# Optimization experiments

Measured on AMD Instinct MI355X. Metric: run time of the kernel, lower is better.

## Reference

```python
import jax, jax.numpy as jnp
import numpy as np

N, E = 20000, 320000
IN_DIM, H, C, L = 256, 128, 40, 3
EPS = 1e-5


def _ln(x, g, b):
    mu = jnp.mean(x, axis=-1, keepdims=True)
    var = jnp.mean(jnp.square(x - mu), axis=-1, keepdims=True)
    return (x - mu) * jax.lax.rsqrt(var + EPS) * g + b


def setup_inputs() -> dict:
    key = jax.random.key(0)
    ks = jax.random.split(key, 24)
    s = lambda *sh: 1.0 / np.sqrt(sh[-2] if len(sh) > 1 else sh[-1])
    inp = {
        "x": jax.random.normal(ks[0], (N, IN_DIM), jnp.float32),
        "edge_index": jax.random.randint(ks[1], (2, E), 0, N, jnp.int32),
        "proj_W": jax.random.normal(ks[2], (IN_DIM, H), jnp.float32) / np.sqrt(IN_DIM),
        "proj_b": jnp.zeros((H,), jnp.float32),
        "ln0_g": jnp.ones((H,), jnp.float32),
        "ln0_b": jnp.zeros((H,), jnp.float32),
        "sim_W1": jax.random.normal(ks[3], (L, 3 * H, H), jnp.float32) / np.sqrt(3 * H),
        "sim_b1": jnp.zeros((L, H), jnp.float32),
        "sim_W2": jax.random.normal(ks[4], (L, H, 1), jnp.float32) / np.sqrt(H),
        "sim_b2": jnp.zeros((L, 1), jnp.float32),
        "W_msg": jax.random.normal(ks[5], (L, H, H), jnp.float32) / np.sqrt(H),
        "W_upd": jax.random.normal(ks[6], (L, 2 * H, H), jnp.float32) / np.sqrt(2 * H),
        "b_upd": jnp.zeros((L, H), jnp.float32),
        "ln_g": jnp.ones((L, H), jnp.float32),
        "ln_b": jnp.zeros((L, H), jnp.float32),
        "cls_W1": jax.random.normal(ks[7], (H, H // 2), jnp.float32) / np.sqrt(H),
        "cls_b1": jnp.zeros((H // 2,), jnp.float32),
        "cls_W2": jax.random.normal(ks[8], (H // 2, C), jnp.float32) / np.sqrt(H // 2),
        "cls_b2": jnp.zeros((C,), jnp.float32),
    }
    return inp


def reference(x, edge_index, proj_W, proj_b, ln0_g, ln0_b, sim_W1, sim_b1,
              sim_W2, sim_b2, W_msg, W_upd, b_upd, ln_g, ln_b,
              cls_W1, cls_b1, cls_W2, cls_b2):
    n = x.shape[0]
    # add self loops
    loops = jnp.arange(n, dtype=edge_index.dtype)
    src = jnp.concatenate([edge_index[0], loops])
    dst = jnp.concatenate([edge_index[1], loops])

    h = jax.nn.relu(_ln(x @ proj_W + proj_b, ln0_g, ln0_b))  # (N,H); dropout=eval no-op

    for l in range(L):
        x_i = h[dst]                      # (E',H)
        x_j = h[src]                      # (E',H)
        sim_in = jnp.concatenate([x_i, x_j, jnp.abs(x_i - x_j)], axis=-1)  # (E',3H)
        hmid = jax.nn.relu(sim_in @ sim_W1[l] + sim_b1[l])
        score = jax.nn.sigmoid(hmid @ sim_W2[l] + sim_b2[l])  # (E',1)
        msg = x_j @ W_msg[l]              # (E',H)
        agg = jax.ops.segment_sum(score * msg, dst, num_segments=n)  # (N,H)
        upd = jnp.concatenate([h, agg], axis=-1) @ W_upd[l] + b_upd[l]
        upd = upd + h                     # residual (identity since in==out)
        h = jax.nn.relu(_ln(upd, ln_g[l], ln_b[l]))

    logits = jax.nn.relu(h @ cls_W1 + cls_b1) @ cls_W2 + cls_b2
    return logits
```

## Files before the change

### kernel.cpp

```cpp
#include <hip/hip_runtime.h>
#include <hip/hip_bf16.h>

#define HD 128
#define LN_EPS 1e-5f

typedef __attribute__((ext_vector_type(8))) short short8;
typedef __attribute__((ext_vector_type(4))) float f32x4;

__device__ __forceinline__ unsigned short f2bf(float f) {
    union { float f; unsigned u; } v; v.f = f;
    unsigned r = (v.u + 0x7fffu + ((v.u >> 16) & 1u)) >> 16;
    return (unsigned short)r;
}

__device__ __forceinline__ unsigned cvtpk(float lo, float hi) {
    unsigned r;
    asm("v_cvt_pk_bf16_f32 %0, %1, %2" : "=v"(r) : "v"(lo), "v"(hi));
    return r;
}
__device__ __forceinline__ unsigned cvtpk_abs(float lo, float hi) {
    unsigned r;
    asm("v_cvt_pk_bf16_f32 %0, abs(%1), abs(%2)" : "=v"(r) : "v"(lo), "v"(hi));
    return r;
}
__device__ __forceinline__ unsigned absd_bf2(unsigned a, unsigned b) {
    float alo = __uint_as_float(a << 16), ahi = __uint_as_float(a & 0xffff0000u);
    float blo = __uint_as_float(b << 16), bhi = __uint_as_float(b & 0xffff0000u);
    return cvtpk_abs(alo - blo, ahi - bhi);
}
__device__ __forceinline__ float bflo(unsigned u) { return __uint_as_float(u << 16); }
__device__ __forceinline__ float bfhi(unsigned u) { return __uint_as_float(u & 0xffff0000u); }

__device__ __forceinline__ float wave_sum_all(float v) {
    #pragma unroll
    for (int o = 32; o > 0; o >>= 1) v += __shfl_xor(v, o);
    return v;
}

__global__ __launch_bounds__(256) void w1bf_kernel(
    const float* __restrict__ W1, unsigned short* __restrict__ out, int total)
{
    int idx = blockIdx.x * 256 + threadIdx.x;
    if (idx >= total) return;
    int lw  = idx / 49152;
    int rem = idx - lw * 49152;
    int j  = rem & 7;
    int c  = (rem >> 3) & 15;
    int ks = (rem >> 7) & 3;
    int ct = (rem >> 9) & 7;
    int q  = rem >> 12;
    out[idx] = f2bf(W1[(size_t)lw * 49152 + (size_t)(q * 32 + ks * 8 + j) * 128 + ct * 16 + c]);
}

__global__ __launch_bounds__(256) void wcbf_kernel(
    const float* __restrict__ W_upd, const float* __restrict__ wcomb2,
    unsigned short* __restrict__ out, int total)
{
    int idx = blockIdx.x * 256 + threadIdx.x;
    if (idx >= total) return;
    int lw  = idx >> 15;
    int rem = idx & 32767;
    int j  = rem & 7;
    int c  = (rem >> 3) & 15;
    int ks = (rem >> 7) & 3;
    int ct = (rem >> 9) & 7;
    int q  = rem >> 12;
    int row = q * 32 + ks * 8 + j;
    int col = ct * 16 + c;
    float v = (row < 128) ? W_upd[(size_t)lw * 32768 + (size_t)row * 128 + col]
                          : wcomb2[(size_t)lw * 16384 + (size_t)(row - 128) * 128 + col];
    out[idx] = f2bf(v);
}

__global__ __launch_bounds__(256) void wmsg_gemm_kernel(
    const float* __restrict__ W_msg, const float* __restrict__ W_upd,
    float* __restrict__ wcomb2)
{
    __shared__ __align__(16) float rows[4][8][128];
    int l   = blockIdx.x >> 2;
    int blk = blockIdx.x & 3;
    const float* A = W_msg + (size_t)l * 16384;
    const float* W = W_upd + (size_t)l * 32768 + 16384;
    float* out = wcomb2 + (size_t)l * 16384;
    int tid = threadIdx.x, wv = tid >> 6, lane = tid & 63;
    int rbase = (blk * 4 + wv) * 8;
    int r = lane >> 3, seg = lane & 7;
    {
        const float2* p = (const float2*)(A + (size_t)(rbase + r) * 128 + seg * 16);
        float2* q = (float2*)&rows[wv][r][seg * 16];
        #pragma unroll
        for (int i = 0; i < 8; i++) q[i] = p[i];
    }
    asm volatile("s_waitcnt lgkmcnt(0)" ::: "memory");
    float2 acc[8];
    #pragma unroll
    for (int t = 0; t < 8; t++) acc[t] = make_float2(0.f, 0.f);
    for (int k = 0; k < 128; k += 4) {
        float2 w0 = *(const float2*)(W + (size_t)(k + 0) * 128 + 2 * lane);
        float2 w1 = *(const float2*)(W + (size_t)(k + 1) * 128 + 2 * lane);
        float2 w2 = *(const float2*)(W + (size_t)(k + 2) * 128 + 2 * lane);
        float2 w3 = *(const float2*)(W + (size_t)(k + 3) * 128 + 2 * lane);
        #pragma unroll
        for (int t = 0; t < 8; t++) {
            float4 a = *(const float4*)&rows[wv][t][k];
            acc[t].x = fmaf(a.x, w0.x, acc[t].x); acc[t].y = fmaf(a.x, w0.y, acc[t].y);
            acc[t].x = fmaf(a.y, w1.x, acc[t].x); acc[t].y = fmaf(a.y, w1.y, acc[t].y);
            acc[t].x = fmaf(a.z, w2.x, acc[t].x); acc[t].y = fmaf(a.z, w2.y, acc[t].y);
            acc[t].x = fmaf(a.w, w3.x, acc[t].x); acc[t].y = fmaf(a.w, w3.y, acc[t].y);
        }
    }
    #pragma unroll
    for (int t = 0; t < 8; t++)
        *(float2*)(out + (size_t)(rbase + t) * 128 + 2 * lane) = acc[t];
}

__global__ __launch_bounds__(256) void gemm_rows_kernel(
    const float* __restrict__ in0, int s0, const float* __restrict__ in1, int s1,
    const float* __restrict__ W, const float* __restrict__ bias,
    const float* __restrict__ res, const float* __restrict__ g,
    const float* __restrict__ bln, float* __restrict__ out,
    unsigned* __restrict__ out_bf, int N)
{
    __shared__ __align__(16) float rows[4][8][256];
    int tid = threadIdx.x, wv = tid >> 6, lane = tid & 63;
    int rbase = (blockIdx.x * 4 + wv) * 8;
    if (rbase >= N) return;
    int K = in1 ? 256 : 128;
    int r = lane >> 3, seg = lane & 7;
    int row = min(rbase + r, N - 1);
    {
        const float4* p = (const float4*)(in0 + (size_t)row * s0 + seg * 16);
        float4* q = (float4*)&rows[wv][r][seg * 16];
        #pragma unroll
        for (int i = 0; i < 4; i++) q[i] = p[i];
        if (in1) {
            const float4* p1 = (const float4*)(in1 + (size_t)row * s1 + seg * 16);
            float4* q1 = (float4*)&rows[wv][r][128 + seg * 16];
            #pragma unroll
            for (int i = 0; i < 4; i++) q1[i] = p1[i];
        }
    }
    asm volatile("s_waitcnt lgkmcnt(0)" ::: "memory");
    float2 acc[8];
    float2 bv = make_float2(0.f, 0.f);
    if (bias) bv = *(const float2*)(bias + 2 * lane);
    #pragma unroll
    for (int t = 0; t < 8; t++) acc[t] = bv;
    for (int k = 0; k < K; k += 4) {
        float2 w0 = *(const float2*)(W + (size_t)(k + 0) * 128 + 2 * lane);
        float2 w1 = *(const float2*)(W + (size_t)(k + 1) * 128 + 2 * lane);
        float2 w2 = *(const float2*)(W + (size_t)(k + 2) * 128 + 2 * lane);
        float2 w3 = *(const float2*)(W + (size_t)(k + 3) * 128 + 2 * lane);
        #pragma unroll
        for (int t = 0; t < 8; t++) {
            float4 a = *(const float4*)&rows[wv][t][k];
            acc[t].x = fmaf(a.x, w0.x, acc[t].x); acc[t].y = fmaf(a.x, w0.y, acc[t].y);
            acc[t].x = fmaf(a.y, w1.x, acc[t].x); acc[t].y = fmaf(a.y, w1.y, acc[t].y);
            acc[t].x = fmaf(a.z, w2.x, acc[t].x); acc[t].y = fmaf(a.z, w2.y, acc[t].y);
            acc[t].x = fmaf(a.w, w3.x, acc[t].x); acc[t].y = fmaf(a.w, w3.y, acc[t].y);
        }
    }
    if (res) {
        #pragma unroll
        for (int t = 0; t < 8; t++) {
            int rw = rbase + t;
            if (rw < N) {
                float2 rv = *(const float2*)(res + (size_t)rw * 128 + 2 * lane);
                acc[t].x += rv.x; acc[t].y += rv.y;
            }
        }
    }
    if (g) {
        float2 gv = *(const float2*)(g + 2 * lane);
        float2 lv = *(const float2*)(bln + 2 * lane);
        #pragma unroll
        for (int t = 0; t < 8; t++) {
            int rw = rbase + t;
            if (rw >= N) break;
            float s  = wave_sum_all(acc[t].x + acc[t].y);
            float s2 = wave_sum_all(acc[t].x * acc[t].x + acc[t].y * acc[t].y);
            float mu = s * (1.f / 128.f);
            float var = s2 * (1.f / 128.f) - mu * mu;
            float rs = rsqrtf(var + LN_EPS);
            float2 y;
            y.x = fmaxf((acc[t].x - mu) * rs * gv.x + lv.x, 0.f);
            y.y = fmaxf((acc[t].y - mu) * rs * gv.y + lv.y, 0.f);
            *(float2*)(out + (size_t)rw * 128 + 2 * lane) = y;
            if (out_bf) out_bf[(size_t)rw * 64 + lane] = cvtpk(y.x, y.y);
        }
    } else {
        #pragma unroll
        for (int t = 0; t < 8; t++) {
            int rw = rbase + t;
            if (rw < N) *(float2*)(out + (size_t)rw * 128 + 2 * lane) = acc[t];
        }
    }
}

__global__ __launch_bounds__(256) void hist_kernel(
    const int* __restrict__ dstA, int* __restrict__ cnt, int E, int Etot)
{
    for (int e = blockIdx.x * 256 + threadIdx.x; e < Etot; e += gridDim.x * 256) {
        int di = (e < E) ? dstA[e] : (e - E);
        atomicAdd(&cnt[di], 1);
    }
}

__global__ __launch_bounds__(256) void scan_kernel(
    const int* __restrict__ cnt, int* __restrict__ rowptr, int* __restrict__ cursor,
    int N, int Etot)
{
    __shared__ int ls[256];
    int t = threadIdx.x;
    int chunk = (N + 255) / 256;
    int lo = t * chunk, hi = min(lo + chunk, N);
    int s = 0;
    for (int i = lo; i < hi; i++) s += cnt[i];
    ls[t] = s;
    __syncthreads();
    for (int off = 1; off < 256; off <<= 1) {
        int v = (t >= off) ? ls[t - off] : 0;
        __syncthreads();
        ls[t] += v;
        __syncthreads();
    }
    int run = ls[t] - s;
    for (int i = lo; i < hi; i++) {
        rowptr[i] = run; cursor[i] = run;
        run += cnt[i];
    }
    if (t == 0) rowptr[N] = Etot;
}

__global__ __launch_bounds__(256) void scatter_kernel(
    const int* __restrict__ srcA, const int* __restrict__ dstA,
    int* __restrict__ cursor, int* __restrict__ esrc, int* __restrict__ edst,
    int E, int Etot)
{
    for (int e = blockIdx.x * 256 + threadIdx.x; e < Etot; e += gridDim.x * 256) {
        int si = (e < E) ? srcA[e] : (e - E);
        int di = (e < E) ? dstA[e] : (e - E);
        int pos = atomicAdd(&cursor[di], 1);
        esrc[pos] = si;
        edst[pos] = di;
    }
}

__global__ __launch_bounds__(256, 3) void edge_mfma_kernel(
    const unsigned* __restrict__ hbf,
    const int* __restrict__ esrc, const int* __restrict__ edst,
    const unsigned short* __restrict__ w1bf, const float* __restrict__ b1,
    const float* __restrict__ W2, const float* __restrict__ b2p,
    float* __restrict__ score, int Etot)
{
    __shared__ __align__(16) short sim[3][64][128];
    __shared__ float pl[4][64];
    int tid = threadIdx.x, wv = tid >> 6, lane = tid & 63;
    char* simb = (char*)sim;

    short8 wf[12][2];
    {
        int ks = lane >> 4, c = lane & 15;
        #pragma unroll
        for (int q = 0; q < 12; q++)
            #pragma unroll
            for (int n = 0; n < 2; n++) {
                int ct = wv * 2 + n;
                wf[q][n] = *(const short8*)(w1bf + (size_t)(((q * 8 + ct) * 4 + ks) * 128 + c * 8));
            }
    }
    float b1x = b1[wv * 32 + (lane & 15)],  b1y = b1[wv * 32 + 16 + (lane & 15)];
    float w2x = W2[wv * 32 + (lane & 15)],  w2y = W2[wv * 32 + 16 + (lane & 15)];
    float b2 = b2p[0];

    int nb = gridDim.x;
    int swz = (blockIdx.x & 7) * (nb >> 3) + (blockIdx.x >> 3);
    int ntiles = (Etot + 63) >> 6;
    int t0 = (int)(((long long)ntiles * swz) / nb);
    int t1 = (int)(((long long)ntiles * (swz + 1)) / nb);
    if (t0 >= t1) return;

    int el = tid >> 2, seg = tid & 3;
    int e_cur = min((t0 << 6) + el, Etot - 1);
    int si = esrc[e_cur];
    int di = edst[e_cur];

    for (int tile = t0; tile < t1; tile++) {
        const uint4* xi = (const uint4*)(hbf + (size_t)di * 64 + seg * 16);
        const uint4* xj = (const uint4*)(hbf + (size_t)si * 64 + seg * 16);
        uint4 a0 = xi[0], b0 = xj[0];
        uint4 a1 = xi[1], b1v = xj[1];
        uint4 a2 = xi[2], b2v = xj[2];
        uint4 a3 = xi[3], b3v = xj[3];
        {
            int nt = (tile + 1 < t1) ? (tile + 1) : tile;
            int en = min((nt << 6) + el, Etot - 1);
            si = esrc[en];
            di = edst[en];
        }
        {
            int rowoff = el * 256, sw = (el & 7) << 4;
            uint4 d0, d1, d2, d3;
            d0.x = absd_bf2(a0.x, b0.x);  d0.y = absd_bf2(a0.y, b0.y);
            d0.z = absd_bf2(a0.z, b0.z);  d0.w = absd_bf2(a0.w, b0.w);
            d1.x = absd_bf2(a1.x, b1v.x); d1.y = absd_bf2(a1.y, b1v.y);
            d1.z = absd_bf2(a1.z, b1v.z); d1.w = absd_bf2(a1.w, b1v.w);
            d2.x = absd_bf2(a2.x, b2v.x); d2.y = absd_bf2(a2.y, b2v.y);
            d2.z = absd_bf2(a2.z, b2v.z); d2.w = absd_bf2(a2.w, b2v.w);
            d3.x = absd_bf2(a3.x, b3v.x); d3.y = absd_bf2(a3.y, b3v.y);
            d3.z = absd_bf2(a3.z, b3v.z); d3.w = absd_bf2(a3.w, b3v.w);
            int o0 = rowoff + ((seg * 64 +  0) ^ sw);
            int o1 = rowoff + ((seg * 64 + 16) ^ sw);
            int o2 = rowoff + ((seg * 64 + 32) ^ sw);
            int o3 = rowoff + ((seg * 64 + 48) ^ sw);
            *(uint4*)(simb + o0)         = a0;  *(uint4*)(simb + o1)         = a1;
            *(uint4*)(simb + o2)         = a2;  *(uint4*)(simb + o3)         = a3;
            *(uint4*)(simb + 16384 + o0) = b0;  *(uint4*)(simb + 16384 + o1) = b1v;
            *(uint4*)(simb + 16384 + o2) = b2v; *(uint4*)(simb + 16384 + o3) = b3v;
            *(uint4*)(simb + 32768 + o0) = d0;  *(uint4*)(simb + 32768 + o1) = d1;
            *(uint4*)(simb + 32768 + o2) = d2;  *(uint4*)(simb + 32768 + o3) = d3;
        }
        __syncthreads();
        f32x4 acc[4][2];
        #pragma unroll
        for (int m = 0; m < 4; m++)
            #pragma unroll
            for (int n = 0; n < 2; n++)
                #pragma unroll
                for (int r = 0; r < 4; r++) acc[m][n][r] = 0.f;
        __builtin_amdgcn_s_setprio(1);
        #pragma unroll
        for (int q = 0; q < 12; q++) {
            int third = q >> 2;
            int kin = ((q & 3) * 64 + (lane >> 4) * 16);
            short8 af[4];
            #pragma unroll
            for (int m = 0; m < 4; m++) {
                int elr = m * 16 + (lane & 15);
                int addr = third * 16384 + elr * 256 + (kin ^ ((elr & 7) << 4));
                af[m] = *(const short8*)(simb + addr);
            }
            #pragma unroll
            for (int m = 0; m < 4; m++)
                #pragma unroll
                for (int n = 0; n < 2; n++)
                    acc[m][n] = __builtin_amdgcn_mfma_f32_16x16x32_bf16(af[m], wf[q][n], acc[m][n], 0, 0, 0);
        }
        __builtin_amdgcn_s_setprio(0);
        int ebase = tile << 6;
        #pragma unroll
        for (int m = 0; m < 4; m++) {
            #pragma unroll
            for (int r = 0; r < 4; r++) {
                float v = fmaxf(acc[m][0][r] + b1x, 0.f) * w2x
                        + fmaxf(acc[m][1][r] + b1y, 0.f) * w2y;
                v += __shfl_xor(v, 1); v += __shfl_xor(v, 2);
                v += __shfl_xor(v, 4); v += __shfl_xor(v, 8);
                if ((lane & 15) == 0) pl[wv][m * 16 + (lane >> 4) * 4 + r] = v;
            }
        }
        __syncthreads();
        if (tid < 64) {
            int e = ebase + tid;
            if (e < Etot) {
                float z = pl[0][tid] + pl[1][tid] + pl[2][tid] + pl[3][tid] + b2;
                score[e] = 1.f / (1.f + __expf(-z));
            }
        }
    }
}

__global__ __launch_bounds__(256) void gather_kernel(
    const int* __restrict__ rowptr, const int* __restrict__ esrc,
    const float* __restrict__ score, const unsigned* __restrict__ hbf,
    unsigned* __restrict__ paggbf, int N)
{
    int nb = gridDim.x;
    int bid = blockIdx.x;
    int swz = (bid & 7) * (nb >> 3) + (bid >> 3);
    int wvi = threadIdx.x >> 6, lane = threadIdx.x & 63;
    int node = swz * 4 + wvi;
    if (node >= N) return;
    int p0 = rowptr[node], p1 = rowptr[node + 1];
    int half = lane >> 5, l32 = lane & 31;
    const uint2* hb2 = (const uint2*)hbf;
    float4 c0 = make_float4(0.f, 0.f, 0.f, 0.f), c1 = c0, c2 = c0, c3 = c0;
    for (int base = p0; base < p1; base += 64) {
        int cnt = min(64, p1 - base);
        int sidx = 0; float sc = 0.f;
        if (lane < cnt) {
            sidx = esrc[base + lane];
            sc = score[base + lane];
        }
        for (int i = 0; i < cnt; i += 8) {
            int j0 = i + 0 + half, j1 = i + 2 + half, j2 = i + 4 + half, j3 = i + 6 + half;
            float s0 = __shfl(sc, j0), s1 = __shfl(sc, j1);
            float s2 = __shfl(sc, j2), s3 = __shfl(sc, j3);
            int r0 = __shfl(sidx, j0), r1 = __shfl(sidx, j1);
            int r2 = __shfl(sidx, j2), r3 = __shfl(sidx, j3);
            if (j0 >= cnt) s0 = 0.f;
            if (j1 >= cnt) s1 = 0.f;
            if (j2 >= cnt) s2 = 0.f;
            if (j3 >= cnt) s3 = 0.f;
            uint2 u0 = hb2[(size_t)r0 * 32 + l32];
            uint2 u1 = hb2[(size_t)r1 * 32 + l32];
            uint2 u2 = hb2[(size_t)r2 * 32 + l32];
            uint2 u3 = hb2[(size_t)r3 * 32 + l32];
            c0.x = fmaf(s0, bflo(u0.x), c0.x); c0.y = fmaf(s0, bfhi(u0.x), c0.y);
            c0.z = fmaf(s0, bflo(u0.y), c0.z); c0.w = fmaf(s0, bfhi(u0.y), c0.w);
            c1.x = fmaf(s1, bflo(u1.x), c1.x); c1.y = fmaf(s1, bfhi(u1.x), c1.y);
            c1.z = fmaf(s1, bflo(u1.y), c1.z); c1.w = fmaf(s1, bfhi(u1.y), c1.w);
            c2.x = fmaf(s2, bflo(u2.x), c2.x); c2.y = fmaf(s2, bfhi(u2.x), c2.y);
            c2.z = fmaf(s2, bflo(u2.y), c2.z); c2.w = fmaf(s2, bfhi(u2.y), c2.w);
            c3.x = fmaf(s3, bflo(u3.x), c3.x); c3.y = fmaf(s3, bfhi(u3.x), c3.y);
            c3.z = fmaf(s3, bflo(u3.y), c3.z); c3.w = fmaf(s3, bfhi(u3.y), c3.w);
        }
    }
    float4 t;
    t.x = (c0.x + c1.x) + (c2.x + c3.x);
    t.y = (c0.y + c1.y) + (c2.y + c3.y);
    t.z = (c0.z + c1.z) + (c2.z + c3.z);
    t.w = (c0.w + c1.w) + (c2.w + c3.w);
    t.x += __shfl_xor(t.x, 32);
    t.y += __shfl_xor(t.y, 32);
    t.z += __shfl_xor(t.z, 32);
    t.w += __shfl_xor(t.w, 32);
    if (half == 0) {
        uint2 o;
        o.x = cvtpk(t.x, t.y);
        o.y = cvtpk(t.z, t.w);
        ((uint2*)paggbf)[(size_t)node * 32 + l32] = o;
    }
}

__global__ __launch_bounds__(256, 3) void upd_mfma_kernel(
    const unsigned* __restrict__ hbf, const unsigned* __restrict__ paggbf,
    const float* __restrict__ hres,
    const unsigned short* __restrict__ wcbf,
    const float* __restrict__ bias, const float* __restrict__ g,
    const float* __restrict__ bln,
    float* __restrict__ hout, unsigned* __restrict__ hbf_out, int N)
{
    __shared__ float ps[4][64], pq[4][64];
    int tid = threadIdx.x, wv = tid >> 6, lane = tid & 63;
    int c = lane & 15, l16 = lane >> 4;
    int rbase = blockIdx.x * 64;
    if (rbase >= N) return;

    short8 wf[8][2];
    #pragma unroll
    for (int q = 0; q < 8; q++)
        #pragma unroll
        for (int n = 0; n < 2; n++) {
            int ct = wv * 2 + n;
            wf[q][n] = *(const short8*)(wcbf + (size_t)(((q * 8 + ct) * 4 + l16) * 128 + c * 8));
        }
    float g0  = g[wv * 32 + c],    g1  = g[wv * 32 + 16 + c];
    float lb0 = bln[wv * 32 + c],  lb1 = bln[wv * 32 + 16 + c];
    float bs0 = bias[wv * 32 + c], bs1 = bias[wv * 32 + 16 + c];

    f32x4 acc[4][2];
    #pragma unroll
    for (int m = 0; m < 4; m++)
        #pragma unroll
        for (int n = 0; n < 2; n++)
            #pragma unroll
            for (int r = 0; r < 4; r++) acc[m][n][r] = 0.f;

    int arow[4];
    #pragma unroll
    for (int m = 0; m < 4; m++) arow[m] = min(rbase + m * 16 + c, N - 1);

    #pragma unroll
    for (int q = 0; q < 8; q++) {
        const unsigned* src = (q < 4) ? hbf : paggbf;
        int qq = (q < 4) ? q : q - 4;
        short8 af[4];
        #pragma unroll
        for (int m = 0; m < 4; m++)
            af[m] = *(const short8*)(src + (size_t)arow[m] * 64 + qq * 16 + l16 * 4);
        #pragma unroll
        for (int m = 0; m < 4; m++)
            #pragma unroll
            for (int n = 0; n < 2; n++)
                acc[m][n] = __builtin_amdgcn_mfma_f32_16x16x32_bf16(af[m], wf[q][n], acc[m][n], 0, 0, 0);
    }

    #pragma unroll
    for (int m = 0; m < 4; m++) {
        #pragma unroll
        for (int r = 0; r < 4; r++) {
            int rit = m * 16 + l16 * 4 + r;
            int rowc = min(rbase + rit, N - 1);
            float v0 = acc[m][0][r] + bs0 + hres[(size_t)rowc * 128 + wv * 32 + c];
            float v1 = acc[m][1][r] + bs1 + hres[(size_t)rowc * 128 + wv * 32 + 16 + c];
            acc[m][0][r] = v0; acc[m][1][r] = v1;
            float s = v0 + v1, sq = v0 * v0 + v1 * v1;
            s  += __shfl_xor(s, 1);  s  += __shfl_xor(s, 2);  s  += __shfl_xor(s, 4);  s  += __shfl_xor(s, 8);
            sq += __shfl_xor(sq, 1); sq += __shfl_xor(sq, 2); sq += __shfl_xor(sq, 4); sq += __shfl_xor(sq, 8);
            if (c == 0) { ps[wv][rit] = s; pq[wv][rit] = sq; }
        }
    }
    __syncthreads();
    #pragma unroll
    for (int m = 0; m < 4; m++) {
        #pragma unroll
        for (int r = 0; r < 4; r++) {
            int rit = m * 16 + l16 * 4 + r;
            int row = rbase + rit;
            float s  = (ps[0][rit] + ps[1][rit]) + (ps[2][rit] + ps[3][rit]);
            float sq = (pq[0][rit] + pq[1][rit]) + (pq[2][rit] + pq[3][rit]);
            float mu = s * (1.f / 128.f);
            float var = sq * (1.f / 128.f) - mu * mu;
            float rs = rsqrtf(var + LN_EPS);
            float y0 = fmaxf((acc[m][0][r] - mu) * rs * g0 + lb0, 0.f);
            float y1 = fmaxf((acc[m][1][r] - mu) * rs * g1 + lb1, 0.f);
            float z0 = __shfl_xor(y0, 1);
            float z1 = __shfl_xor(y1, 1);
            if (row < N) {
                hout[(size_t)row * 128 + wv * 32 + c]      = y0;
                hout[(size_t)row * 128 + wv * 32 + 16 + c] = y1;
                if (!(lane & 1)) {
                    hbf_out[(size_t)row * 64 + wv * 16 + (c >> 1)]     = cvtpk(y0, z0);
                    hbf_out[(size_t)row * 64 + wv * 16 + 8 + (c >> 1)] = cvtpk(y1, z1);
                }
            }
        }
    }
}

__global__ __launch_bounds__(256) void cls_kernel(
    const float* __restrict__ hin, const float* __restrict__ W1,
    const float* __restrict__ b1, const float* __restrict__ W2,
    const float* __restrict__ b2, float* __restrict__ out, int N)
{
    __shared__ __align__(16) float w1[HD * 64];
    __shared__ __align__(16) float w2[64 * 40];
    __shared__ __align__(16) float hs[4][HD];
    __shared__ float ts[4][64];
    for (int i = threadIdx.x; i < HD * 64; i += 256) w1[i] = W1[i];
    for (int i = threadIdx.x; i < 64 * 40; i += 256) w2[i] = W2[i];
    int sub = threadIdx.x >> 6, t = threadIdx.x & 63;
    float b1j = b1[t];
    float b2j = (t < 40) ? b2[t] : 0.f;
    __syncthreads();
    for (int base = blockIdx.x * 4; base < N; base += gridDim.x * 4) {
        int i = base + sub; bool val = i < N;
        if (val) { hs[sub][t] = hin[(size_t)i * HD + t]; hs[sub][64 + t] = hin[(size_t)i * HD + 64 + t]; }
        __syncthreads();
        float acc = b1j;
        const float* hr = hs[sub];
        #pragma unroll 8
        for (int k = 0; k < HD; k += 4) {
            float4 hv = *(const float4*)(hr + k);
            acc = fmaf(hv.x, w1[(k + 0) * 64 + t], acc);
            acc = fmaf(hv.y, w1[(k + 1) * 64 + t], acc);
            acc = fmaf(hv.z, w1[(k + 2) * 64 + t], acc);
            acc = fmaf(hv.w, w1[(k + 3) * 64 + t], acc);
        }
        ts[sub][t] = fmaxf(acc, 0.f);
        __syncthreads();
        if (val && t < 40) {
            float o = b2j;
            const float* tr = ts[sub];
            #pragma unroll 8
            for (int k = 0; k < 64; k++) o = fmaf(tr[k], w2[k * 40 + t], o);
            out[(size_t)i * 40 + t] = o;
        }
        __syncthreads();
    }
}

extern "C" void kernel_launch(void* const* d_in, const int* in_sizes, int n_in,
                              void* d_out, int out_size, void* d_ws, size_t ws_size,
                              hipStream_t stream)
{
    const float* x      = (const float*)d_in[0];
    const int*   ei     = (const int*)d_in[1];
    const float* proj_W = (const float*)d_in[2];
    const float* proj_b = (const float*)d_in[3];
    const float* ln0_g  = (const float*)d_in[4];
    const float* ln0_b  = (const float*)d_in[5];
    const float* sim_W1 = (const float*)d_in[6];
    const float* sim_b1 = (const float*)d_in[7];
    const float* sim_W2 = (const float*)d_in[8];
    const float* sim_b2 = (const float*)d_in[9];
    const float* W_msg  = (const float*)d_in[10];
    const float* W_upd  = (const float*)d_in[11];
    const float* b_upd  = (const float*)d_in[12];
    const float* ln_g   = (const float*)d_in[13];
    const float* ln_b   = (const float*)d_in[14];
    const float* cls_W1 = (const float*)d_in[15];
    const float* cls_b1 = (const float*)d_in[16];
    const float* cls_W2 = (const float*)d_in[17];
    const float* cls_b2 = (const float*)d_in[18];

    int N = in_sizes[0] / 256;
    int E = in_sizes[1] / 2;
    int L = in_sizes[6] / (3 * HD * HD);
    int Etot = E + N;
    const int* srcA = ei;
    const int* dstA = ei + E;

    float* ws = (float*)d_ws;
    size_t nh = (size_t)N * HD;
    float* h      = ws;
    float* score  = h + nh;
    float* wcomb2 = score + Etot + 64;
    unsigned* hbf    = (unsigned*)(wcomb2 + (size_t)L * 16384);
    unsigned* paggbf = hbf + nh / 2;
    unsigned short* w1bf = (unsigned short*)(paggbf + nh / 2);
    unsigned short* wcbf = w1bf + (size_t)L * 49152;
    int*   cnt    = (int*)(wcbf + (size_t)L * 32768);
    int*   rowptr = cnt + N;
    int*   cursor = rowptr + N + 1;
    int*   esrc   = cursor + N;
    int*   edst   = esrc + Etot;

    int gemm_blocks = (N + 31) / 32;

    hipMemsetAsync(cnt, 0, (size_t)N * sizeof(int), stream);
    hist_kernel<<<512, 256, 0, stream>>>(dstA, cnt, E, Etot);
    scan_kernel<<<1, 256, 0, stream>>>(cnt, rowptr, cursor, N, Etot);
    scatter_kernel<<<512, 256, 0, stream>>>(srcA, dstA, cursor, esrc, edst, E, Etot);

    int w1_total = L * 49152;
    w1bf_kernel<<<(w1_total + 255) / 256, 256, 0, stream>>>(sim_W1, w1bf, w1_total);

    wmsg_gemm_kernel<<<4 * L, 256, 0, stream>>>(W_msg, W_upd, wcomb2);
    int wc_total = L * 32768;
    wcbf_kernel<<<(wc_total + 255) / 256, 256, 0, stream>>>(W_upd, wcomb2, wcbf, wc_total);

    gemm_rows_kernel<<<gemm_blocks, 256, 0, stream>>>(x, 256, x + 128, 256, proj_W, proj_b,
                                                      nullptr, ln0_g, ln0_b, h, hbf, N);

    int gather_blocks = (N + 3) / 4;
    int upd_blocks = (N + 63) / 64;
    for (int l = 0; l < L; l++) {
        edge_mfma_kernel<<<768, 256, 0, stream>>>(hbf, esrc, edst,
                                                  w1bf + (size_t)l * 49152, sim_b1 + l * HD,
                                                  sim_W2 + l * HD, sim_b2 + l, score, Etot);
        gather_kernel<<<gather_blocks, 256, 0, stream>>>(rowptr, esrc, score, hbf, paggbf, N);
        upd_mfma_kernel<<<upd_blocks, 256, 0, stream>>>(hbf, paggbf, h,
                                                        wcbf + (size_t)l * 32768,
                                                        b_upd + l * HD, ln_g + l * HD, ln_b + l * HD,
                                                        h, hbf, N);
    }
    cls_kernel<<<768, 256, 0, stream>>>(h, cls_W1, cls_b1, cls_W2, cls_b2, (float*)d_out, N);
}
```

Before: 420.7 us.

## Load edge MFMA operands directly from global memory instead of staging in LDS

The edge similarity kernel no longer stages x_i, x_j and |x_i-x_j| for a 64-edge tile through shared memory. Edge indices are broadcast across lanes with shuffles, and each wave loads its bf16 A-fragments straight from the node feature table in MFMA layout. The absolute difference is computed in registers. This removes the LDS writes and reads and the pre-MFMA barrier. The cost is that all four waves of a block now fetch the same edge rows, quadrupling global/L2 gather traffic, and an extra barrier is needed to protect the partial-sum buffer.

Result: slower. 569.2 us (+35.3%).

```diff
diff --git a/kernel.cpp b/kernel.cpp
--- a/kernel.cpp
+++ b/kernel.cpp
@@ -6,6 +6,8 @@
 
 typedef __attribute__((ext_vector_type(8))) short short8;
 typedef __attribute__((ext_vector_type(4))) float f32x4;
+
+union U4S8 { uint4 u; short8 s; };
 
 __device__ __forceinline__ unsigned short f2bf(float f) {
     union { float f; unsigned u; } v; v.f = f;
@@ -253,24 +255,22 @@
     const float* __restrict__ W2, const float* __restrict__ b2p,
     float* __restrict__ score, int Etot)
 {
-    __shared__ __align__(16) short sim[3][64][128];
     __shared__ float pl[4][64];
     int tid = threadIdx.x, wv = tid >> 6, lane = tid & 63;
-    char* simb = (char*)sim;
+    int c = lane & 15, l16 = lane >> 4;
 
     short8 wf[12][2];
     {
-        int ks = lane >> 4, c = lane & 15;
         #pragma unroll
         for (int q = 0; q < 12; q++)
             #pragma unroll
             for (int n = 0; n < 2; n++) {
                 int ct = wv * 2 + n;
-                wf[q][n] = *(const short8*)(w1bf + (size_t)(((q * 8 + ct) * 4 + ks) * 128 + c * 8));
-            }
-    }
-    float b1x = b1[wv * 32 + (lane & 15)],  b1y = b1[wv * 32 + 16 + (lane & 15)];
-    float w2x = W2[wv * 32 + (lane & 15)],  w2y = W2[wv * 32 + 16 + (lane & 15)];
+                wf[q][n] = *(const short8*)(w1bf + (size_t)(((q * 8 + ct) * 4 + l16) * 128 + c * 8));
+            }
+    }
+    float b1x = b1[wv * 32 + c],  b1y = b1[wv * 32 + 16 + c];
+    float w2x = W2[wv * 32 + c],  w2y = W2[wv * 32 + 16 + c];
     float b2 = b2p[0];
 
     int nb = gridDim.x;
@@ -280,47 +280,23 @@
     int t1 = (int)(((long long)ntiles * (swz + 1)) / nb);
     if (t0 >= t1) return;
 
-    int el = tid >> 2, seg = tid & 3;
-    int e_cur = min((t0 << 6) + el, Etot - 1);
-    int si = esrc[e_cur];
-    int di = edst[e_cur];
+    int e_l = min((t0 << 6) + lane, Etot - 1);
+    int si_all = esrc[e_l];
+    int di_all = edst[e_l];
 
     for (int tile = t0; tile < t1; tile++) {
-        const uint4* xi = (const uint4*)(hbf + (size_t)di * 64 + seg * 16);
-        const uint4* xj = (const uint4*)(hbf + (size_t)si * 64 + seg * 16);
-        uint4 a0 = xi[0], b0 = xj[0];
-        uint4 a1 = xi[1], b1v = xj[1];
-        uint4 a2 = xi[2], b2v = xj[2];
-        uint4 a3 = xi[3], b3v = xj[3];
+        int sim_[4], dim_[4];
+        #pragma unroll
+        for (int m = 0; m < 4; m++) {
+            sim_[m] = __shfl(si_all, m * 16 + c);
+            dim_[m] = __shfl(di_all, m * 16 + c);
+        }
         {
             int nt = (tile + 1 < t1) ? (tile + 1) : tile;
-            int en = min((nt << 6) + el, Etot - 1);
-            si = esrc[en];
-            di = edst[en];
-        }
-        {
-            int rowoff = el * 256, sw = (el & 7) << 4;
-            uint4 d0, d1, d2, d3;
-            d0.x = absd_bf2(a0.x, b0.x);  d0.y = absd_bf2(a0.y, b0.y);
-            d0.z = absd_bf2(a0.z, b0.z);  d0.w = absd_bf2(a0.w, b0.w);
-            d1.x = absd_bf2(a1.x, b1v.x); d1.y = absd_bf2(a1.y, b1v.y);
-            d1.z = absd_bf2(a1.z, b1v.z); d1.w = absd_bf2(a1.w, b1v.w);
-            d2.x = absd_bf2(a2.x, b2v.x); d2.y = absd_bf2(a2.y, b2v.y);
-            d2.z = absd_bf2(a2.z, b2v.z); d2.w = absd_bf2(a2.w, b2v.w);
-            d3.x = absd_bf2(a3.x, b3v.x); d3.y = absd_bf2(a3.y, b3v.y);
-            d3.z = absd_bf2(a3.z, b3v.z); d3.w = absd_bf2(a3.w, b3v.w);
-            int o0 = rowoff + ((seg * 64 +  0) ^ sw);
-            int o1 = rowoff + ((seg * 64 + 16) ^ sw);
-            int o2 = rowoff + ((seg * 64 + 32) ^ sw);
-            int o3 = rowoff + ((seg * 64 + 48) ^ sw);
-            *(uint4*)(simb + o0)         = a0;  *(uint4*)(simb + o1)         = a1;
-            *(uint4*)(simb + o2)         = a2;  *(uint4*)(simb + o3)         = a3;
-            *(uint4*)(simb + 16384 + o0) = b0;  *(uint4*)(simb + 16384 + o1) = b1v;
-            *(uint4*)(simb + 16384 + o2) = b2v; *(uint4*)(simb + 16384 + o3) = b3v;
-            *(uint4*)(simb + 32768 + o0) = d0;  *(uint4*)(simb + 32768 + o1) = d1;
-            *(uint4*)(simb + 32768 + o2) = d2;  *(uint4*)(simb + 32768 + o3) = d3;
-        }
-        __syncthreads();
+            int en = min((nt << 6) + lane, Etot - 1);
+            si_all = esrc[en];
+            di_all = edst[en];
+        }
         f32x4 acc[4][2];
         #pragma unroll
         for (int m = 0; m < 4; m++)
@@ -328,26 +304,38 @@
             for (int n = 0; n < 2; n++)
                 #pragma unroll
                 for (int r = 0; r < 4; r++) acc[m][n][r] = 0.f;
-        __builtin_amdgcn_s_setprio(1);
-        #pragma unroll
-        for (int q = 0; q < 12; q++) {
-            int third = q >> 2;
-            int kin = ((q & 3) * 64 + (lane >> 4) * 16);
-            short8 af[4];
+
+        #pragma unroll
+        for (int q = 0; q < 4; q++) {
+            int off = q * 16 + l16 * 4;
+            U4S8 ai[4], aj[4];
+            #pragma unroll
+            for (int m = 0; m < 4; m++) ai[m].u = *(const uint4*)(hbf + (size_t)dim_[m] * 64 + off);
+            #pragma unroll
+            for (int m = 0; m < 4; m++) aj[m].u = *(const uint4*)(hbf + (size_t)sim_[m] * 64 + off);
+            __builtin_amdgcn_s_setprio(1);
             #pragma unroll
             for (int m = 0; m < 4; m++) {
-                int elr = m * 16 + (lane & 15);
-                int addr = third * 16384 + elr * 256 + (kin ^ ((elr & 7) << 4));
-                af[m] = *(const short8*)(simb + addr);
-            }
-            #pragma unroll
-            for (int m = 0; m < 4; m++)
-                #pragma unroll
-                for (int n = 0; n < 2; n++)
-                    acc[m][n] = __builtin_amdgcn_mfma_f32_16x16x32_bf16(af[m], wf[q][n], acc[m][n], 0, 0, 0);
-        }
-        __builtin_amdgcn_s_setprio(0);
-        int ebase = tile << 6;
+                acc[m][0] = __builtin_amdgcn_mfma_f32_16x16x32_bf16(ai[m].s, wf[q][0], acc[m][0], 0, 0, 0);
+                acc[m][1] = __builtin_amdgcn_mfma_f32_16x16x32_bf16(ai[m].s, wf[q][1], acc[m][1], 0, 0, 0);
+            }
+            #pragma unroll
+            for (int m = 0; m < 4; m++) {
+                acc[m][0] = __builtin_amdgcn_mfma_f32_16x16x32_bf16(aj[m].s, wf[4 + q][0], acc[m][0], 0, 0, 0);
+                acc[m][1] = __builtin_amdgcn_mfma_f32_16x16x32_bf16(aj[m].s, wf[4 + q][1], acc[m][1], 0, 0, 0);
+            }
+            #pragma unroll
+            for (int m = 0; m < 4; m++) {
+                U4S8 d;
+                d.u.x = absd_bf2(ai[m].u.x, aj[m].u.x);
+                d.u.y = absd_bf2(ai[m].u.y, aj[m].u.y);
+                d.u.z = absd_bf2(ai[m].u.z, aj[m].u.z);
+                d.u.w = absd_bf2(ai[m].u.w, aj[m].u.w);
+                acc[m][0] = __builtin_amdgcn_mfma_f32_16x16x32_bf16(d.s, wf[8 + q][0], acc[m][0], 0, 0, 0);
+                acc[m][1] = __builtin_amdgcn_mfma_f32_16x16x32_bf16(d.s, wf[8 + q][1], acc[m][1], 0, 0, 0);
+            }
+            __builtin_amdgcn_s_setprio(0);
+        }
         #pragma unroll
         for (int m = 0; m < 4; m++) {
             #pragma unroll
@@ -356,17 +344,18 @@
                         + fmaxf(acc[m][1][r] + b1y, 0.f) * w2y;
                 v += __shfl_xor(v, 1); v += __shfl_xor(v, 2);
                 v += __shfl_xor(v, 4); v += __shfl_xor(v, 8);
-                if ((lane & 15) == 0) pl[wv][m * 16 + (lane >> 4) * 4 + r] = v;
+                if (c == 0) pl[wv][m * 16 + l16 * 4 + r] = v;
             }
         }
         __syncthreads();
         if (tid < 64) {
-            int e = ebase + tid;
+            int e = (tile << 6) + tid;
             if (e < Etot) {
                 float z = pl[0][tid] + pl[1][tid] + pl[2][tid] + pl[3][tid] + b2;
                 score[e] = 1.f / (1.f + __expf(-z));
             }
         }
+        __syncthreads();
     }
 }
 
```
